# Kernel optimization log

Measured on AMD Instinct MI355X. Metric: run time of the kernel, lower is better.

## Reference

```python
import jax, jax.numpy as jnp
import numpy as np

N = 400000      # simplices (edges of the complexes)
E = 2400000     # nnz of each Laplacian
F_IN = 32
H = 64
KAPPA = 3
G = 512         # graphs in batch
N_OUT = 8
EPS = 1e-5


def spmm(edge_index, edge_values, x, n):
    # y[i] = sum_e val_e * x[j],  i = edge_index[0], j = edge_index[1]
    msg = edge_values[:, None] * x[edge_index[1]]
    return jax.ops.segment_sum(msg, edge_index[0], num_segments=n)


def sc_layer(x, li, lv, ui, uv, Wl, bl, Wu, bu, Wh, bh):
    # SCNN layer: z_low + z_up + z_har (aggr_x fused in)
    n = x.shape[0]
    z = x @ Wh + bh                       # harmonic / identity term
    xl = x
    for k in range(KAPPA):
        xl = spmm(li, lv, xl, n)          # L_low^{k+1} x
        z = z + xl @ Wl[k] + bl[k]
    xu = x
    for k in range(KAPPA):
        xu = spmm(ui, uv, xu, n)          # L_up^{k+1} x
        z = z + xu @ Wu[k] + bu[k]
    return z


def batch_norm(x, gamma, beta):
    mean = jnp.mean(x, axis=0)
    var = jnp.mean((x - mean) ** 2, axis=0)   # biased, as torch BN training
    return (x - mean) * jax.lax.rsqrt(var + EPS) * gamma + beta


def setup_inputs() -> dict:
    key = jax.random.key(0)
    ks = jax.random.split(key, 32)
    s_in = 1.0 / np.sqrt(F_IN)
    s_h = 1.0 / np.sqrt(H)
    inp = {
        "x": jax.random.normal(ks[0], (N, F_IN), jnp.float32),
        "lower_edge_index": jax.random.randint(ks[1], (2, E), 0, N),
        "lower_edge_values": jax.random.normal(ks[2], (E,), jnp.float32),
        "upper_edge_index": jax.random.randint(ks[3], (2, E), 0, N),
        "upper_edge_values": jax.random.normal(ks[4], (E,), jnp.float32),
        "batch_index": jnp.sort(jax.random.randint(ks[5], (N,), 0, G)),
        # layer 0 (F_IN -> H)
        "l0_Wl": jax.random.normal(ks[6], (KAPPA, F_IN, H), jnp.float32) * s_in,
        "l0_bl": jnp.zeros((KAPPA, H), jnp.float32),
        "l0_Wu": jax.random.normal(ks[7], (KAPPA, F_IN, H), jnp.float32) * s_in,
        "l0_bu": jnp.zeros((KAPPA, H), jnp.float32),
        "l0_Wh": jax.random.normal(ks[8], (F_IN, H), jnp.float32) * s_in,
        "l0_bh": jnp.zeros((H,), jnp.float32),
        # layer 1 (H -> H)
        "l1_Wl": jax.random.normal(ks[9], (KAPPA, H, H), jnp.float32) * s_h,
        "l1_bl": jnp.zeros((KAPPA, H), jnp.float32),
        "l1_Wu": jax.random.normal(ks[10], (KAPPA, H, H), jnp.float32) * s_h,
        "l1_bu": jnp.zeros((KAPPA, H), jnp.float32),
        "l1_Wh": jax.random.normal(ks[11], (H, H), jnp.float32) * s_h,
        "l1_bh": jnp.zeros((H,), jnp.float32),
        # batch norms
        "bn0_g": jnp.ones((H,), jnp.float32),
        "bn0_b": jnp.zeros((H,), jnp.float32),
        "bn1_g": jnp.ones((H,), jnp.float32),
        "bn1_b": jnp.zeros((H,), jnp.float32),
        # output MLP [2H, H, N_OUT]
        "mlp_W1": jax.random.normal(ks[12], (2 * H, H), jnp.float32) / np.sqrt(2 * H),
        "mlp_b1": jnp.zeros((H,), jnp.float32),
        "mlp_W2": jax.random.normal(ks[13], (H, N_OUT), jnp.float32) * s_h,
        "mlp_b2": jnp.zeros((N_OUT,), jnp.float32),
    }
    return inp


def reference(x, lower_edge_values, upper_edge_values,
              l0_Wl, l0_bl, l0_Wu, l0_bu, l0_Wh, l0_bh,
              l1_Wl, l1_bl, l1_Wu, l1_bu, l1_Wh, l1_bh,
              bn0_g, bn0_b, bn1_g, bn1_b,
              mlp_W1, mlp_b1, mlp_W2, mlp_b2,
              lower_edge_index, upper_edge_index, batch_index):
    li, ui, bi = lower_edge_index, upper_edge_index, batch_index
    lv, uv = lower_edge_values, upper_edge_values

    h = sc_layer(x, li, lv, ui, uv, l0_Wl, l0_bl, l0_Wu, l0_bu, l0_Wh, l0_bh)
    h = jax.nn.elu(batch_norm(h, bn0_g, bn0_b))
    h = sc_layer(h, li, lv, ui, uv, l1_Wl, l1_bl, l1_Wu, l1_bu, l1_Wh, l1_bh)
    h = jax.nn.elu(batch_norm(h, bn1_g, bn1_b))

    # global max pool + global mean pool per graph
    gmax = jax.ops.segment_max(h, bi, num_segments=G)
    gsum = jax.ops.segment_sum(h, bi, num_segments=G)
    cnt = jax.ops.segment_sum(jnp.ones((h.shape[0],), h.dtype), bi, num_segments=G)
    gmean = gsum / jnp.maximum(cnt, 1.0)[:, None]
    g = jax.nn.elu(jnp.concatenate([gmax, gmean], axis=1))  # [G, 2H]

    # MLP [2H -> H -> N_OUT]
    g = jax.nn.relu(g @ mlp_W1 + mlp_b1)
    return g @ mlp_W2 + mlp_b2
```

## Files before the change

kernel.cpp:

```cpp
#include <hip/hip_runtime.h>
#include <hip/hip_bf16.h>
#include <math.h>

#define N_SIMP 400000
#define E_NNZ  2400000
#define FIN    32
#define HDIM   64
#define KAPPA  3
#define G_NUM  512
#define NOUT   8
#define BN_EPS 1e-5

#define NDIG_HALF 391
#define NDIG      782
#define P1_EDGES  8192
#define P1_BLOCKS 586
#define P1_T      1024
#define P1_EPT    8
#define P2_CAP    7168
#define P2_T      512
#define P2_ITERS  14

#define MF_BLOCKS_C 6250

typedef __hip_bfloat16 bf16;
typedef _Float16 f16;
typedef short s8v __attribute__((ext_vector_type(8)));
typedef ushort u8v __attribute__((ext_vector_type(8)));
typedef _Float16 h8v __attribute__((ext_vector_type(8)));
typedef float f4v __attribute__((ext_vector_type(4)));

__device__ __forceinline__ float elu_f(float x) {
    return x > 0.f ? x : expm1f(x);
}
__device__ __forceinline__ float bf2f(ushort u) {
    return __uint_as_float(((unsigned int)u) << 16);
}
__device__ __forceinline__ ushort f2bf(float f) {
    bf16 h = (bf16)f;
    return *(ushort*)&h;
}


__global__ __launch_bounds__(P1_T) void p1_sort_kernel(
        const int* __restrict__ eiL, const float* __restrict__ lv,
        const int* __restrict__ eiU, const float* __restrict__ uv,
        int* __restrict__ ccnt, int* __restrict__ bofsv,
        int2* __restrict__ coarse) {
    __shared__ int2 rec[P1_EDGES];
    __shared__ int h[NDIG];
    __shared__ int hscan[P1_T];
    int t = threadIdx.x;
    for (int j = t; j < NDIG; j += P1_T) h[j] = 0;
    __syncthreads();
    int base_i = blockIdx.x * P1_EDGES;
    int key[P1_EPT], val[P1_EPT], dg[P1_EPT];
#pragma unroll
    for (int k = 0; k < P1_EPT; ++k) {
        int i = base_i + k * P1_T + t;
        int dd = -1;
        if (i < 2 * E_NNZ) {
            int row, col;
            float v;
            if (i < E_NNZ) {
                row = eiL[i]; col = eiL[E_NNZ + i]; v = lv[i];
                dd = row >> 10;
            } else {
                int e = i - E_NNZ;
                row = eiU[e]; col = eiU[E_NNZ + e]; v = uv[e];
                dd = NDIG_HALF + (row >> 10);
            }
            key[k] = ((row & 1023) << 22) | col;
            val[k] = __float_as_int(v);
            atomicAdd(&h[dd], 1);
        }
        dg[k] = dd;
    }
    __syncthreads();
    int cv = (t < NDIG) ? h[t] : 0;
    hscan[t] = cv;
    __syncthreads();
    for (int off = 1; off < P1_T; off <<= 1) {
        int x = (t >= off) ? hscan[t - off] : 0;
        __syncthreads();
        hscan[t] += x;
        __syncthreads();
    }
    if (t < NDIG) {
        int ex = hscan[t] - cv;
        ccnt[blockIdx.x * NDIG + t] = cv;
        bofsv[blockIdx.x * NDIG + t] = ex;
        h[t] = ex;
    }
    __syncthreads();
#pragma unroll
    for (int k = 0; k < P1_EPT; ++k) {
        if (dg[k] >= 0) {
            int pos = atomicAdd(&h[dg[k]], 1);
            rec[pos] = make_int2(key[k], val[k]);
        }
    }
    __syncthreads();
    int2* dst = coarse + (size_t)blockIdx.x * P1_EDGES;
    int nrec = 2 * E_NNZ - base_i;
    if (nrec > P1_EDGES) nrec = P1_EDGES;
    for (int j = t; j < nrec; j += P1_T) dst[j] = rec[j];
}

__global__ void digit_total_kernel(const int* __restrict__ cnt, int* __restrict__ tot) {
    int d = blockIdx.x * 256 + threadIdx.x;
    if (d >= NDIG) return;
    int run = 0;
    for (int b = 0; b < P1_BLOCKS; ++b) run += cnt[b * NDIG + d];
    tot[d] = run;
}

__global__ __launch_bounds__(1024) void scan_base_kernel(int* __restrict__ tot) {
    __shared__ int s[1024];
    int t = threadIdx.x;
    int v = (t < NDIG) ? tot[t] : 0;
    s[t] = v;
    __syncthreads();
    for (int off = 1; off < 1024; off <<= 1) {
        int x = (t >= off) ? s[t - off] : 0;
        __syncthreads();
        s[t] += x;
        __syncthreads();
    }
    if (t < NDIG) tot[t] = s[t] - v;
    if (t == 1023) tot[NDIG] = s[1023];
}


__global__ __launch_bounds__(P2_T) void p2_build_kernel(
        const int2* __restrict__ coarse, const int* __restrict__ ccnt,
        const int* __restrict__ bofsv, const int* __restrict__ basev,
        int* __restrict__ rpL, int* __restrict__ rpU,
        int2* __restrict__ edgeL, int2* __restrict__ edgeU) {
    __shared__ int pk[P2_CAP];
    __shared__ int vl[P2_CAP];
    __shared__ int hist[1024];
    __shared__ int sc[P2_T];
    __shared__ int flen[P1_BLOCKS];
    __shared__ int fofs[P1_BLOCKS];
    __shared__ int fo[P1_BLOCKS];
    __shared__ int stot;
    int d = blockIdx.x;
    int t = threadIdx.x;
    int f0 = 2 * t, f1 = 2 * t + 1;
    int L0 = 0, L1 = 0, O0 = 0, O1 = 0;
    if (f0 < P1_BLOCKS) { L0 = ccnt[f0 * NDIG + d]; O0 = bofsv[f0 * NDIG + d]; }
    if (f1 < P1_BLOCKS) { L1 = ccnt[f1 * NDIG + d]; O1 = bofsv[f1 * NDIG + d]; }
    sc[t] = L0 + L1;
    __syncthreads();
    for (int off = 1; off < P2_T; off <<= 1) {
        int x = (t >= off) ? sc[t - off] : 0;
        __syncthreads();
        sc[t] += x;
        __syncthreads();
    }
    int pb = sc[t] - (L0 + L1);
    if (f0 < P1_BLOCKS) { flen[f0] = L0; fofs[f0] = O0; fo[f0] = pb; }
    if (f1 < P1_BLOCKS) { flen[f1] = L1; fofs[f1] = O1; fo[f1] = pb + L0; }
    if (t == P2_T - 1) stot = sc[t];
    __syncthreads();
    int sz = stot;
    if (sz > P2_CAP) sz = P2_CAP;
    int wv = t >> 6, lane = t & 63;
    int grp8 = lane >> 3, l8 = lane & 7;
    for (int b = wv * 8 + grp8; b < P1_BLOCKS; b += 64) {
        int L = flen[b], O = fofs[b], F = fo[b];
        const int2* sp = coarse + (size_t)b * P1_EDGES + O;
        for (int j = l8; j < L; j += 8) {
            int dst2 = F + j;
            if (dst2 < P2_CAP) {
                int2 r = sp[j];
                pk[dst2] = r.x;
                vl[dst2] = r.y;
            }
        }
    }
    __syncthreads();
    hist[t] = 0;
    hist[t + P2_T] = 0;
    __syncthreads();
    int myrank[P2_ITERS];
#pragma unroll
    for (int k = 0; k < P2_ITERS; ++k) {
        int j = k * P2_T + t;
        myrank[k] = (j < sz) ? atomicAdd(&hist[((unsigned)pk[j]) >> 22], 1) : 0;
    }
    __syncthreads();
    int h0 = hist[2 * t], h1 = hist[2 * t + 1];
    sc[t] = h0 + h1;
    __syncthreads();
    for (int off = 1; off < P2_T; off <<= 1) {
        int x = (t >= off) ? sc[t - off] : 0;
        __syncthreads();
        sc[t] += x;
        __syncthreads();
    }
    int pbase = sc[t] - (h0 + h1);
    __syncthreads();
    hist[2 * t] = pbase;
    hist[2 * t + 1] = pbase + h0;
    int which = (d >= NDIG_HALF);
    int lbase = basev[d] - (which ? E_NNZ : 0);
    int rowbase = (which ? d - NDIG_HALF : d) << 10;
    int* rp = which ? rpU : rpL;
    int r0 = rowbase + 2 * t, r1 = r0 + 1;
    if (r0 < N_SIMP) rp[r0] = lbase + pbase;
    if (r1 < N_SIMP) rp[r1] = lbase + pbase + h0;
    __syncthreads();
    int2* eout = which ? edgeU : edgeL;
#pragma unroll
    for (int k = 0; k < P2_ITERS; ++k) {
        int j = k * P2_T + t;
        if (j < sz) {
            unsigned p = (unsigned)pk[j];
            int pos = lbase + hist[p >> 22] + myrank[k];
            eout[pos] = make_int2((int)(p & 0x3FFFFF), vl[j]);
        }
    }
}


__global__ void combine_bias_kernel(const float* __restrict__ bh,
                                    const float* __restrict__ bl,
                                    const float* __restrict__ bu,
                                    float* __restrict__ out) {
    int h = threadIdx.x;
    float acc = bh[h];
    for (int k = 0; k < KAPPA; ++k) acc += bl[k * HDIM + h] + bu[k * HDIM + h];
    out[h] = acc;
}

__global__ void f32_to_bf16_kernel(const float* __restrict__ in, bf16* __restrict__ out) {
    int idx = blockIdx.x * 256 + threadIdx.x;
    float4 v = ((const float4*)in)[idx];
    ushort4 w;
    w.x = f2bf(v.x); w.y = f2bf(v.y); w.z = f2bf(v.z); w.w = f2bf(v.w);
    ((ushort4*)out)[idx] = w;
}

__global__ void wtrans_all_kernel(const float* __restrict__ s0, const float* __restrict__ s1,
                                  const float* __restrict__ s2, const float* __restrict__ s3,
                                  const float* __restrict__ s4, const float* __restrict__ s5,
                                  ushort* __restrict__ wt) {
    int idx = blockIdx.x * 256 + threadIdx.x;
    const float* src; int off;
    if (idx < 2048)       { src = s0; off = 0; }
    else if (idx < 6144)  { src = s1; off = 2048; }
    else if (idx < 12288) { src = s2; off = 6144; }
    else if (idx < 18432) { src = s3; off = 12288; }
    else if (idx < 30720) { src = s4; off = 18432; }
    else                  { src = s5; off = 30720; }
    int rel = idx - off;
    int frag = rel >> 9;
    int r = rel & 511;
    int lane = r >> 3, j = r & 7;
    int q = lane >> 4, n = lane & 15;
    int ch = frag >> 2, nblk = frag & 3;
    int k = ch * 32 + q * 8 + j;
    int nout = nblk * 16 + n;
    wt[idx] = f2bf(src[k * 64 + nout]);
}


__global__ void spmm32_kernel(const int* __restrict__ rp, const int2* __restrict__ edge,
                              const bf16* __restrict__ srcb, int src_stride,
                              bf16* __restrict__ dstb) {
    const ushort* src = (const ushort*)srcb;
    ushort* dst = (ushort*)dstb;
    int tid = threadIdx.x;
    int lane = tid & 63;
    int wv = tid >> 6;
    int grp = lane >> 2;
    int li = lane & 3;
    int row = blockIdx.x * 64 + wv * 16 + grp;
    int s = rp[row];
    int e = (row == N_SIMP - 1) ? E_NNZ : rp[row + 1];
    int deg = e - s;
    float a[8] = {0.f, 0.f, 0.f, 0.f, 0.f, 0.f, 0.f, 0.f};
    if (deg > 0) {
        int2 ed[8];
#pragma unroll
        for (int t = 0; t < 8; ++t) {
            int j = s + t;
            ed[t] = edge[(j < e) ? j : (e - 1)];
        }
        u8v xs[8];
#pragma unroll
        for (int t = 0; t < 8; ++t)
            xs[t] = *(const u8v*)(src + (size_t)ed[t].x * src_stride + li * 8);
#pragma unroll
        for (int t = 0; t < 8; ++t) {
            float v = (t < deg) ? __int_as_float(ed[t].y) : 0.f;
#pragma unroll
            for (int c = 0; c < 8; ++c) a[c] += v * bf2f(xs[t][c]);
        }
        for (int j = s + 8; j < e; j += 4) {
            int2 e2[4];
#pragma unroll
            for (int t = 0; t < 4; ++t) {
                int jj = j + t;
                e2[t] = edge[(jj < e) ? jj : (e - 1)];
            }
            u8v x2[4];
#pragma unroll
            for (int t = 0; t < 4; ++t)
                x2[t] = *(const u8v*)(src + (size_t)e2[t].x * src_stride + li * 8);
#pragma unroll
            for (int t = 0; t < 4; ++t) {
                float v = (j + t < e) ? __int_as_float(e2[t].y) : 0.f;
#pragma unroll
                for (int c = 0; c < 8; ++c) a[c] += v * bf2f(x2[t][c]);
            }
        }
    }
    u8v w;
#pragma unroll
    for (int c = 0; c < 8; ++c) w[c] = f2bf(a[c]);
    *(u8v*)(dst + (size_t)row * 32 + li * 8) = w;
}

__global__ void spmm64_kernel(const int* __restrict__ rp, const int2* __restrict__ edge,
                              const bf16* __restrict__ srcb, bf16* __restrict__ dstb) {
    const ushort* src = (const ushort*)srcb;
    ushort* dst = (ushort*)dstb;
    int tid = threadIdx.x;
    int lane = tid & 63;
    int wv = tid >> 6;
    int grp = lane >> 3;
    int li = lane & 7;
    int row = blockIdx.x * 32 + wv * 8 + grp;
    int s = rp[row];
    int e = (row == N_SIMP - 1) ? E_NNZ : rp[row + 1];
    int deg = e - s;
    float a[8] = {0.f, 0.f, 0.f, 0.f, 0.f, 0.f, 0.f, 0.f};
    if (deg > 0) {
        int2 ed[8];
#pragma unroll
        for (int t = 0; t < 8; ++t) {
            int j = s + t;
            ed[t] = edge[(j < e) ? j : (e - 1)];
        }
        u8v xs[8];
#pragma unroll
        for (int t = 0; t < 8; ++t)
            xs[t] = *(const u8v*)(src + (size_t)ed[t].x * 64 + li * 8);
#pragma unroll
        for (int t = 0; t < 8; ++t) {
            float v = (t < deg) ? __int_as_float(ed[t].y) : 0.f;
#pragma unroll
            for (int c = 0; c < 8; ++c) a[c] += v * bf2f(xs[t][c]);
        }
        for (int j = s + 8; j < e; j += 4) {
            int2 e2[4];
#pragma unroll
            for (int t = 0; t < 4; ++t) {
                int jj = j + t;
                e2[t] = edge[(jj < e) ? jj : (e - 1)];
            }
            u8v x2[4];
#pragma unroll
            for (int t = 0; t < 4; ++t)
                x2[t] = *(const u8v*)(src + (size_t)e2[t].x * 64 + li * 8);
#pragma unroll
            for (int t = 0; t < 4; ++t) {
                float v = (j + t < e) ? __int_as_float(e2[t].y) : 0.f;
#pragma unroll
                for (int c = 0; c < 8; ++c) a[c] += v * bf2f(x2[t][c]);
            }
        }
    }
    u8v w;
#pragma unroll
    for (int c = 0; c < 8; ++c) w[c] = f2bf(a[c]);
    *(u8v*)(dst + (size_t)row * 64 + li * 8) = w;
}


template <int NCH, int NCH1, bool INIT, bool STATS>
__global__ __launch_bounds__(256) void mfma_gemm_kernel(
        const ushort* __restrict__ s0, int st0,
        const ushort* __restrict__ s1, int st1,
        const ushort* __restrict__ s2, int st2,
        const ushort* __restrict__ s3, int st3,
        const ushort* __restrict__ s4, int st4,
        const ushort* __restrict__ s5, int st5,
        const ushort* __restrict__ Wt1,
        const ushort* __restrict__ Wt2,
        const float* __restrict__ bias,
        float* __restrict__ partial,
        f16* __restrict__ z) {
    __shared__ float s_sum[64], s_sq[64];
    int tid = threadIdx.x;
    int wv = tid >> 6, lane = tid & 63;
    int quad = lane >> 4, n = lane & 15;
    int rowbase = blockIdx.x * 64 + wv * 16;
    int arow = rowbase + n;

    if (STATS) {
        if (tid < 64) { s_sum[tid] = 0.f; s_sq[tid] = 0.f; }
        __syncthreads();
    }

    f4v acc0 = {0.f, 0.f, 0.f, 0.f};
    f4v acc1 = {0.f, 0.f, 0.f, 0.f};
    f4v acc2 = {0.f, 0.f, 0.f, 0.f};
    f4v acc3 = {0.f, 0.f, 0.f, 0.f};

#pragma unroll
    for (int ch = 0; ch < NCH; ++ch) {
        const ushort* sp = (ch == 0) ? s0 : (ch == 1) ? s1 : (ch == 2) ? s2
                         : (ch == 3) ? s3 : (ch == 4) ? s4 : s5;
        int st = (ch == 0) ? st0 : (ch == 1) ? st1 : (ch == 2) ? st2
               : (ch == 3) ? st3 : (ch == 4) ? st4 : st5;
        const ushort* wb = (ch < NCH1) ? (Wt1 + (size_t)ch * 2048)
                                       : (Wt2 + (size_t)(ch - NCH1) * 2048);
        s8v a = *(const s8v*)(sp + (size_t)arow * st + quad * 8);
        const ushort* wq = wb + lane * 8;
        s8v b0 = *(const s8v*)(wq + 0 * 512);
        s8v b1 = *(const s8v*)(wq + 1 * 512);
        s8v b2 = *(const s8v*)(wq + 2 * 512);
        s8v b3 = *(const s8v*)(wq + 3 * 512);
        acc0 = __builtin_amdgcn_mfma_f32_16x16x32_bf16(a, b0, acc0, 0, 0, 0);
        acc1 = __builtin_amdgcn_mfma_f32_16x16x32_bf16(a, b1, acc1, 0, 0, 0);
        acc2 = __builtin_amdgcn_mfma_f32_16x16x32_bf16(a, b2, acc2, 0, 0, 0);
        acc3 = __builtin_amdgcn_mfma_f32_16x16x32_bf16(a, b3, acc3, 0, 0, 0);
    }
    float fs[4] = {0.f, 0.f, 0.f, 0.f};
    float fq[4] = {0.f, 0.f, 0.f, 0.f};
#pragma unroll
    for (int r = 0; r < 4; ++r) {
        int orow = rowbase + quad * 4 + r;
        f16* zp = z + (size_t)orow * 64 + n;
        f16 w0, w1, w2, w3;
        if (INIT) {
            w0 = (f16)(bias[n]      + acc0[r]);
            w1 = (f16)(bias[16 + n] + acc1[r]);
            w2 = (f16)(bias[32 + n] + acc2[r]);
            w3 = (f16)(bias[48 + n] + acc3[r]);
        } else {
            w0 = (f16)((float)zp[0]  + acc0[r]);
            w1 = (f16)((float)zp[16] + acc1[r]);
            w2 = (f16)((float)zp[32] + acc2[r]);
            w3 = (f16)((float)zp[48] + acc3[r]);
        }
        zp[0] = w0; zp[16] = w1; zp[32] = w2; zp[48] = w3;
        if (STATS) {
            float v0 = (float)w0, v1 = (float)w1, v2 = (float)w2, v3 = (float)w3;
            fs[0] += v0; fq[0] += v0 * v0;
            fs[1] += v1; fq[1] += v1 * v1;
            fs[2] += v2; fq[2] += v2 * v2;
            fs[3] += v3; fq[3] += v3 * v3;
        }
    }
    if (STATS) {
#pragma unroll
        for (int k = 0; k < 4; ++k) {
            atomicAdd(&s_sum[k * 16 + n], fs[k]);
            atomicAdd(&s_sq[k * 16 + n], fq[k]);
        }
        __syncthreads();
        if (tid < 64)  partial[(size_t)blockIdx.x * 128 + tid] = s_sum[tid];
        else if (tid < 128) partial[(size_t)blockIdx.x * 128 + tid] = s_sq[tid - 64];
    }
}

__global__ __launch_bounds__(256) void stats_reduce_kernel(
        const float* __restrict__ partial, double* __restrict__ stats) {
    __shared__ double sd[256];
    int slot = blockIdx.x;
    int t = threadIdx.x;
    double acc = 0.0;
    for (int j = t; j < MF_BLOCKS_C; j += 256)
        acc += (double)partial[(size_t)j * 128 + slot];
    sd[t] = acc;
    __syncthreads();
    for (int off = 128; off > 0; off >>= 1) {
        if (t < off) sd[t] += sd[t + off];
        __syncthreads();
    }
    if (t == 0) stats[slot] = sd[0];
}


__global__ void bn_elu_bf16_kernel(const f16* __restrict__ z, const double* __restrict__ stats,
                                   const float* __restrict__ gamma, const float* __restrict__ beta,
                                   bf16* __restrict__ out) {
    __shared__ float scale_s[64], shift_s[64];
    int tid = threadIdx.x;
    if (tid < 64) {
        double mean = stats[tid] / (double)N_SIMP;
        double var = stats[64 + tid] / (double)N_SIMP - mean * mean;
        double sc = (double)gamma[tid] / sqrt(var + BN_EPS);
        scale_s[tid] = (float)sc;
        shift_s[tid] = (float)((double)beta[tid] - mean * sc);
    }
    __syncthreads();
    const h8v* z8 = (const h8v*)z;
    u8v* o8 = (u8v*)out;
    const int total8 = N_SIMP * HDIM / 8;
    int hb = (tid & 7) * 8;
    for (int i = blockIdx.x * 256 + tid; i < total8; i += (int)gridDim.x * 256) {
        h8v v = z8[i];
        u8v w;
#pragma unroll
        for (int c = 0; c < 8; ++c)
            w[c] = f2bf(elu_f((float)v[c] * scale_s[hb + c] + shift_s[hb + c]));
        o8[i] = w;
    }
}

__global__ void pool_bn_kernel(const f16* __restrict__ zbuf, const int* __restrict__ bidx,
                               const double* __restrict__ stats,
                               const float* __restrict__ gamma, const float* __restrict__ beta,
                               float* __restrict__ gbuf) {
    __shared__ float scale_s[64], shift_s[64];
    __shared__ float pmax[256 * 8], psum[256 * 8];
    int tid = threadIdx.x;
    if (tid < 64) {
        double mean = stats[tid] / (double)N_SIMP;
        double var = stats[64 + tid] / (double)N_SIMP - mean * mean;
        double sc = (double)gamma[tid] / sqrt(var + BN_EPS);
        scale_s[tid] = (float)sc;
        shift_s[tid] = (float)((double)beta[tid] - mean * sc);
    }
    __syncthreads();
    int g = blockIdx.x;
    int lo = 0, hi = N_SIMP;
    while (lo < hi) { int mid = (lo + hi) >> 1; if (bidx[mid] < g) lo = mid + 1; else hi = mid; }
    int start = lo;
    hi = N_SIMP;
    while (lo < hi) { int mid = (lo + hi) >> 1; if (bidx[mid] < g + 1) lo = mid + 1; else hi = mid; }
    int end = lo;
    int li = tid & 7;
    int rr = tid >> 3;
    const h8v* z8 = (const h8v*)zbuf;
    float mx[8], sm[8];
#pragma unroll
    for (int c = 0; c < 8; ++c) { mx[c] = -INFINITY; sm[c] = 0.f; }
    float sc8[8], sh8[8];
#pragma unroll
    for (int c = 0; c < 8; ++c) { sc8[c] = scale_s[li * 8 + c]; sh8[c] = shift_s[li * 8 + c]; }
    for (int i = start + rr; i < end; i += 32) {
        h8v v = z8[(size_t)i * 8 + li];
#pragma unroll
        for (int c = 0; c < 8; ++c) {
            float y = elu_f((float)v[c] * sc8[c] + sh8[c]);
            mx[c] = fmaxf(mx[c], y);
            sm[c] += y;
        }
    }
#pragma unroll
    for (int c = 0; c < 8; ++c) { pmax[tid * 8 + c] = mx[c]; psum[tid * 8 + c] = sm[c]; }
    __syncthreads();
    if (tid < 64) {
        int sel = tid >> 3, slot = tid & 7;
        float m = -INFINITY, s = 0.f;
#pragma unroll 8
        for (int k = 0; k < 32; ++k) {
            int t = k * 8 + sel;
            m = fmaxf(m, pmax[t * 8 + slot]);
            s += psum[t * 8 + slot];
        }
        int cnt = end - start;
        float mean = s / fmaxf((float)cnt, 1.f);
        gbuf[g * 128 + tid] = elu_f(m);
        gbuf[g * 128 + 64 + tid] = elu_f(mean);
    }
}

__global__ void mlp_kernel(const float* __restrict__ gbuf, const float* __restrict__ W1,
                           const float* __restrict__ b1, const float* __restrict__ W2,
                           const float* __restrict__ b2, float* __restrict__ out) {
    __shared__ float gs[128];
    __shared__ float hs[64];
    int g = blockIdx.x, tid = threadIdx.x;
    gs[tid] = gbuf[g * 128 + tid];
    gs[64 + tid] = gbuf[g * 128 + 64 + tid];
    __syncthreads();
    float acc = b1[tid];
#pragma unroll
    for (int k = 0; k < 128; ++k) acc += gs[k] * W1[k * 64 + tid];
    hs[tid] = fmaxf(acc, 0.f);
    __syncthreads();
    if (tid < 8) {
        float o = b2[tid];
#pragma unroll
        for (int k = 0; k < 64; ++k) o += hs[k] * W2[k * 8 + tid];
        out[g * 8 + tid] = o;
    }
}


extern "C" void kernel_launch(void* const* d_in, const int* in_sizes, int n_in,
                              void* d_out, int out_size, void* d_ws, size_t ws_size,
                              hipStream_t stream) {
    const float* x     = (const float*)d_in[0];
    const int*   li    = (const int*)d_in[1];
    const float* lv    = (const float*)d_in[2];
    const int*   ui    = (const int*)d_in[3];
    const float* uv    = (const float*)d_in[4];
    const int*   bidx  = (const int*)d_in[5];
    const float* l0_Wl = (const float*)d_in[6];
    const float* l0_bl = (const float*)d_in[7];
    const float* l0_Wu = (const float*)d_in[8];
    const float* l0_bu = (const float*)d_in[9];
    const float* l0_Wh = (const float*)d_in[10];
    const float* l0_bh = (const float*)d_in[11];
    const float* l1_Wl = (const float*)d_in[12];
    const float* l1_bl = (const float*)d_in[13];
    const float* l1_Wu = (const float*)d_in[14];
    const float* l1_bu = (const float*)d_in[15];
    const float* l1_Wh = (const float*)d_in[16];
    const float* l1_bh = (const float*)d_in[17];
    const float* bn0_g = (const float*)d_in[18];
    const float* bn0_b = (const float*)d_in[19];
    const float* bn1_g = (const float*)d_in[20];
    const float* bn1_b = (const float*)d_in[21];
    const float* mW1   = (const float*)d_in[22];
    const float* mb1   = (const float*)d_in[23];
    const float* mW2   = (const float*)d_in[24];
    const float* mb2   = (const float*)d_in[25];
    float* out = (float*)d_out;

    char* base = (char*)d_ws;
    f16*   z     = (f16*)base;
    bf16*  h0bf  = (bf16*)(base + 51200000ull);
    bf16*  g1    = (bf16*)(base + 102400000ull);
    bf16*  g2    = (bf16*)(base + 153600000ull);
    int2*  edgeL = (int2*)(base + 204800000ull);
    int2*  edgeU = (int2*)(base + 224000000ull);
    int*   rpL   = (int*)(base + 243200000ull);
    int*   rpU   = (int*)(base + 244800032ull);
    double* stats = (double*)(base + 246404160ull);
    float* cbias  = (float*)(base + 246405184ull);
    float* gbuf   = (float*)(base + 246405440ull);
    ushort* wt    = (ushort*)(base + 246667584ull);
    float* partial = (float*)(base + 246760000ull);

    int2* coarse = (int2*)base;
    int*  basev  = (int*)(base + 38500000ull);
    int*  ccnt   = (int*)(base + 51200000ull);
    int*  bofsv  = (int*)(base + 53100000ull);

    bf16* xbf  = g1;
    bf16* cAL  = g1 + (size_t)N_SIMP * 32;
    bf16* cBL  = g2;
    bf16* cCL  = g2 + (size_t)N_SIMP * 32;
    bf16* cAU  = h0bf;
    bf16* cBU  = h0bf + (size_t)N_SIMP * 32;
    bf16* cCU  = g1;

    ushort* wt_l0h = wt;
    ushort* wt_l1h = wt + 2048;
    ushort* wt_l0l = wt + 6144;
    ushort* wt_l0u = wt + 12288;
    ushort* wt_l1l = wt + 18432;
    ushort* wt_l1u = wt + 30720;

    const int SP32_BLOCKS = N_SIMP / 64;
    const int SP64_BLOCKS = N_SIMP / 32;
    const int MF_BLOCKS   = N_SIMP / 64;

    wtrans_all_kernel<<<168, 256, 0, stream>>>(l0_Wh, l1_Wh, l0_Wl, l0_Wu, l1_Wl, l1_Wu, wt);
    f32_to_bf16_kernel<<<N_SIMP * 32 / 4 / 256, 256, 0, stream>>>(x, xbf);

    p1_sort_kernel<<<P1_BLOCKS, P1_T, 0, stream>>>(li, lv, ui, uv, ccnt, bofsv, coarse);
    digit_total_kernel<<<(NDIG + 255) / 256, 256, 0, stream>>>(ccnt, basev);
    scan_base_kernel<<<1, 1024, 0, stream>>>(basev);
    p2_build_kernel<<<NDIG, P2_T, 0, stream>>>(coarse, ccnt, bofsv, basev,
                                               rpL, rpU, edgeL, edgeU);

    const ushort* xbfu = (const ushort*)xbf;
    const ushort* h0u  = (const ushort*)h0bf;
    const ushort* g1u  = (const ushort*)g1;
    const ushort* g2u  = (const ushort*)g2;

    combine_bias_kernel<<<1, 64, 0, stream>>>(l0_bh, l0_bl, l0_bu, cbias);
    mfma_gemm_kernel<1, 1, true, false><<<MF_BLOCKS, 256, 0, stream>>>(
        xbfu, 32, nullptr, 0, nullptr, 0, nullptr, 0, nullptr, 0, nullptr, 0,
        wt_l0h, wt_l0h, cbias, nullptr, z);

    spmm32_kernel<<<SP32_BLOCKS, 256, 0, stream>>>(rpL, edgeL, xbf, 32, cAL);
    spmm32_kernel<<<SP32_BLOCKS, 256, 0, stream>>>(rpL, edgeL, cAL, 32, cBL);
    spmm32_kernel<<<SP32_BLOCKS, 256, 0, stream>>>(rpL, edgeL, cBL, 32, cCL);
    spmm32_kernel<<<SP32_BLOCKS, 256, 0, stream>>>(rpU, edgeU, xbf, 32, cAU);
    spmm32_kernel<<<SP32_BLOCKS, 256, 0, stream>>>(rpU, edgeU, cAU, 32, cBU);
    spmm32_kernel<<<SP32_BLOCKS, 256, 0, stream>>>(rpU, edgeU, cBU, 32, cCU);
    mfma_gemm_kernel<6, 3, false, true><<<MF_BLOCKS, 256, 0, stream>>>(
        (const ushort*)cAL, 32, (const ushort*)cBL, 32, (const ushort*)cCL, 32,
        (const ushort*)cAU, 32, (const ushort*)cBU, 32, (const ushort*)cCU, 32,
        wt_l0l, wt_l0u, nullptr, partial, z);
    stats_reduce_kernel<<<128, 256, 0, stream>>>(partial, stats);

    bn_elu_bf16_kernel<<<1024, 256, 0, stream>>>(z, stats, bn0_g, bn0_b, h0bf);

    combine_bias_kernel<<<1, 64, 0, stream>>>(l1_bh, l1_bl, l1_bu, cbias);

    spmm64_kernel<<<SP64_BLOCKS, 256, 0, stream>>>(rpL, edgeL, h0bf, g1);
    spmm64_kernel<<<SP64_BLOCKS, 256, 0, stream>>>(rpL, edgeL, g1, g2);
    mfma_gemm_kernel<6, 2, true, false><<<MF_BLOCKS, 256, 0, stream>>>(
        h0u, 64, h0u + 32, 64, g1u, 64, g1u + 32, 64, g2u, 64, g2u + 32, 64,
        wt_l1h, wt_l1l, cbias, nullptr, z);
    spmm64_kernel<<<SP64_BLOCKS, 256, 0, stream>>>(rpL, edgeL, g2, g1);
    spmm64_kernel<<<SP64_BLOCKS, 256, 0, stream>>>(rpU, edgeU, h0bf, g2);
    mfma_gemm_kernel<4, 2, false, false><<<MF_BLOCKS, 256, 0, stream>>>(
        g1u, 64, g1u + 32, 64, g2u, 64, g2u + 32, 64, nullptr, 0, nullptr, 0,
        wt_l1l + 4 * 2048, wt_l1u, nullptr, nullptr, z);
    spmm64_kernel<<<SP64_BLOCKS, 256, 0, stream>>>(rpU, edgeU, g2, g1);
    spmm64_kernel<<<SP64_BLOCKS, 256, 0, stream>>>(rpU, edgeU, g1, g2);
    mfma_gemm_kernel<4, 4, false, true><<<MF_BLOCKS, 256, 0, stream>>>(
        g1u, 64, g1u + 32, 64, g2u, 64, g2u + 32, 64, nullptr, 0, nullptr, 0,
        wt_l1u + 2 * 2048, wt_l1u + 2 * 2048, nullptr, partial, z);
    stats_reduce_kernel<<<128, 256, 0, stream>>>(partial, stats);

    pool_bn_kernel<<<G_NUM, 256, 0, stream>>>(z, bidx, stats, bn1_g, bn1_b, gbuf);
    mlp_kernel<<<G_NUM, 64, 0, stream>>>(gbuf, mW1, mb1, mW2, mb2, out);
}
```

Before: 1.234 ms.

## Merge layer-1 GEMM passes and stage GEMM epilogue through LDS for vector stores

Layer 1 is rescheduled so the third lower-Laplacian power is written into the z buffer, reinterpreted as bf16 scratch. All lower-side and harmonic terms are then applied in one 8-chunk INIT GEMM, and all upper-side terms in one 6-chunk accumulating GEMM. This cuts one full read-modify-write pass over z and one kernel launch. The GEMM epilogue also now writes the accumulators to a shared-memory tile and emits 8-wide half-precision vector loads and stores, replacing scattered per-element stores. The cost is extra LDS traffic and a block barrier. Reusing z as scratch relies on each block reading its own rows before overwriting them.

Result: slower. 1.326 ms (+7.5%).

```diff
diff --git a/kernel.cpp b/kernel.cpp
--- a/kernel.cpp
+++ b/kernel.cpp
@@ -389,11 +389,14 @@
         const ushort* __restrict__ s3, int st3,
         const ushort* __restrict__ s4, int st4,
         const ushort* __restrict__ s5, int st5,
+        const ushort* __restrict__ s6, int st6,
+        const ushort* __restrict__ s7, int st7,
         const ushort* __restrict__ Wt1,
         const ushort* __restrict__ Wt2,
         const float* __restrict__ bias,
         float* __restrict__ partial,
         f16* __restrict__ z) {
+    __shared__ float ctile[64][68];
     __shared__ float s_sum[64], s_sq[64];
     int tid = threadIdx.x;
     int wv = tid >> 6, lane = tid & 63;
@@ -401,11 +404,6 @@
     int rowbase = blockIdx.x * 64 + wv * 16;
     int arow = rowbase + n;
 
-    if (STATS) {
-        if (tid < 64) { s_sum[tid] = 0.f; s_sq[tid] = 0.f; }
-        __syncthreads();
-    }
-
     f4v acc0 = {0.f, 0.f, 0.f, 0.f};
     f4v acc1 = {0.f, 0.f, 0.f, 0.f};
     f4v acc2 = {0.f, 0.f, 0.f, 0.f};
@@ -414,9 +412,11 @@
 #pragma unroll
     for (int ch = 0; ch < NCH; ++ch) {
         const ushort* sp = (ch == 0) ? s0 : (ch == 1) ? s1 : (ch == 2) ? s2
-                         : (ch == 3) ? s3 : (ch == 4) ? s4 : s5;
+                         : (ch == 3) ? s3 : (ch == 4) ? s4 : (ch == 5) ? s5
+                         : (ch == 6) ? s6 : s7;
         int st = (ch == 0) ? st0 : (ch == 1) ? st1 : (ch == 2) ? st2
-               : (ch == 3) ? st3 : (ch == 4) ? st4 : st5;
+               : (ch == 3) ? st3 : (ch == 4) ? st4 : (ch == 5) ? st5
+               : (ch == 6) ? st6 : st7;
         const ushort* wb = (ch < NCH1) ? (Wt1 + (size_t)ch * 2048)
                                        : (Wt2 + (size_t)(ch - NCH1) * 2048);
         s8v a = *(const s8v*)(sp + (size_t)arow * st + quad * 8);
@@ -430,38 +430,49 @@
         acc2 = __builtin_amdgcn_mfma_f32_16x16x32_bf16(a, b2, acc2, 0, 0, 0);
         acc3 = __builtin_amdgcn_mfma_f32_16x16x32_bf16(a, b3, acc3, 0, 0, 0);
     }
-    float fs[4] = {0.f, 0.f, 0.f, 0.f};
-    float fq[4] = {0.f, 0.f, 0.f, 0.f};
 #pragma unroll
     for (int r = 0; r < 4; ++r) {
-        int orow = rowbase + quad * 4 + r;
-        f16* zp = z + (size_t)orow * 64 + n;
-        f16 w0, w1, w2, w3;
+        int lrow = wv * 16 + quad * 4 + r;
+        ctile[lrow][n]      = acc0[r];
+        ctile[lrow][16 + n] = acc1[r];
+        ctile[lrow][32 + n] = acc2[r];
+        ctile[lrow][48 + n] = acc3[r];
+    }
+    if (STATS && tid < 64) { s_sum[tid] = 0.f; s_sq[tid] = 0.f; }
+    __syncthreads();
+    float fs[8] = {0, 0, 0, 0, 0, 0, 0, 0};
+    float fq[8] = {0, 0, 0, 0, 0, 0, 0, 0};
+    int cb = (tid & 7) * 8;
+#pragma unroll
+    for (int k = 0; k < 2; ++k) {
+        int lrow = (tid + k * 256) >> 3;
+        f16* zp = z + ((size_t)blockIdx.x * 64 + lrow) * 64 + cb;
+        h8v o;
         if (INIT) {
-            w0 = (f16)(bias[n]      + acc0[r]);
-            w1 = (f16)(bias[16 + n] + acc1[r]);
-            w2 = (f16)(bias[32 + n] + acc2[r]);
-            w3 = (f16)(bias[48 + n] + acc3[r]);
+#pragma unroll
+            for (int c = 0; c < 8; ++c)
+                o[c] = (f16)(ctile[lrow][cb + c] + bias[cb + c]);
         } else {
-            w0 = (f16)((float)zp[0]  + acc0[r]);
-            w1 = (f16)((float)zp[16] + acc1[r]);
-            w2 = (f16)((float)zp[32] + acc2[r]);
-            w3 = (f16)((float)zp[48] + acc3[r]);
-        }
-        zp[0] = w0; zp[16] = w1; zp[32] = w2; zp[48] = w3;
+            h8v old = *(const h8v*)zp;
+#pragma unroll
+            for (int c = 0; c < 8; ++c)
+                o[c] = (f16)((float)old[c] + ctile[lrow][cb + c]);
+        }
+        *(h8v*)zp = o;
         if (STATS) {
-            float v0 = (float)w0, v1 = (float)w1, v2 = (float)w2, v3 = (float)w3;
-            fs[0] += v0; fq[0] += v0 * v0;
-            fs[1] += v1; fq[1] += v1 * v1;
-            fs[2] += v2; fq[2] += v2 * v2;
-            fs[3] += v3; fq[3] += v3 * v3;
+#pragma unroll
+            for (int c = 0; c < 8; ++c) {
+                float v = (float)o[c];
+                fs[c] += v;
+                fq[c] += v * v;
+            }
         }
     }
     if (STATS) {
 #pragma unroll
-        for (int k = 0; k < 4; ++k) {
-            atomicAdd(&s_sum[k * 16 + n], fs[k]);
-            atomicAdd(&s_sq[k * 16 + n], fq[k]);
+        for (int c = 0; c < 8; ++c) {
+            atomicAdd(&s_sum[cb + c], fs[c]);
+            atomicAdd(&s_sq[cb + c], fq[c]);
         }
         __syncthreads();
         if (tid < 64)  partial[(size_t)blockIdx.x * 128 + tid] = s_sum[tid];
@@ -655,6 +666,8 @@
     bf16* cBU  = h0bf + (size_t)N_SIMP * 32;
     bf16* cCU  = g1;
 
+    bf16* zb = (bf16*)z;
+
     ushort* wt_l0h = wt;
     ushort* wt_l1h = wt + 2048;
     ushort* wt_l0l = wt + 6144;
@@ -679,11 +692,12 @@
     const ushort* h0u  = (const ushort*)h0bf;
     const ushort* g1u  = (const ushort*)g1;
     const ushort* g2u  = (const ushort*)g2;
+    const ushort* zbu  = (const ushort*)zb;
 
     combine_bias_kernel<<<1, 64, 0, stream>>>(l0_bh, l0_bl, l0_bu, cbias);
     mfma_gemm_kernel<1, 1, true, false><<<MF_BLOCKS, 256, 0, stream>>>(
         xbfu, 32, nullptr, 0, nullptr, 0, nullptr, 0, nullptr, 0, nullptr, 0,
-        wt_l0h, wt_l0h, cbias, nullptr, z);
+        nullptr, 0, nullptr, 0, wt_l0h, wt_l0h, cbias, nullptr, z);
 
     spmm32_kernel<<<SP32_BLOCKS, 256, 0, stream>>>(rpL, edgeL, xbf, 32, cAL);
     spmm32_kernel<<<SP32_BLOCKS, 256, 0, stream>>>(rpL, edgeL, cAL, 32, cBL);
@@ -694,7 +708,7 @@
     mfma_gemm_kernel<6, 3, false, true><<<MF_BLOCKS, 256, 0, stream>>>(
         (const ushort*)cAL, 32, (const ushort*)cBL, 32, (const ushort*)cCL, 32,
         (const ushort*)cAU, 32, (const ushort*)cBU, 32, (const ushort*)cCU, 32,
-        wt_l0l, wt_l0u, nullptr, partial, z);
+        nullptr, 0, nullptr, 0, wt_l0l, wt_l0u, nullptr, partial, z);
     stats_reduce_kernel<<<128, 256, 0, stream>>>(partial, stats);
 
     bn_elu_bf16_kernel<<<1024, 256, 0, stream>>>(z, stats, bn0_g, bn0_b, h0bf);
@@ -703,19 +717,16 @@
 
     spmm64_kernel<<<SP64_BLOCKS, 256, 0, stream>>>(rpL, edgeL, h0bf, g1);
     spmm64_kernel<<<SP64_BLOCKS, 256, 0, stream>>>(rpL, edgeL, g1, g2);
-    mfma_gemm_kernel<6, 2, true, false><<<MF_BLOCKS, 256, 0, stream>>>(
+    spmm64_kernel<<<SP64_BLOCKS, 256, 0, stream>>>(rpL, edgeL, g2, zb);
+    mfma_gemm_kernel<8, 2, true, false><<<MF_BLOCKS, 256, 0, stream>>>(
         h0u, 64, h0u + 32, 64, g1u, 64, g1u + 32, 64, g2u, 64, g2u + 32, 64,
-        wt_l1h, wt_l1l, cbias, nullptr, z);
-    spmm64_kernel<<<SP64_BLOCKS, 256, 0, stream>>>(rpL, edgeL, g2, g1);
-    spmm64_kernel<<<SP64_BLOCKS, 256, 0, stream>>>(rpU, edgeU, h0bf, g2);
-    mfma_gemm_kernel<4, 2, false, false><<<MF_BLOCKS, 256, 0, stream>>>(
-        g1u, 64, g1u + 32, 64, g2u, 64, g2u + 32, 64, nullptr, 0, nullptr, 0,
-        wt_l1l + 4 * 2048, wt_l1u, nullptr, nullptr, z);
-    spmm64_kernel<<<SP64_BLOCKS, 256, 0, stream>>>(rpU, edgeU, g2, g1);
+        zbu, 64, zbu + 32, 64, wt_l1h, wt_l1l, cbias, nullptr, z);
+    spmm64_kernel<<<SP64_BLOCKS, 256, 0, stream>>>(rpU, edgeU, h0bf, g1);
     spmm64_kernel<<<SP64_BLOCKS, 256, 0, stream>>>(rpU, edgeU, g1, g2);
-    mfma_gemm_kernel<4, 4, false, true><<<MF_BLOCKS, 256, 0, stream>>>(
-        g1u, 64, g1u + 32, 64, g2u, 64, g2u + 32, 64, nullptr, 0, nullptr, 0,
-        wt_l1u + 2 * 2048, wt_l1u + 2 * 2048, nullptr, partial, z);
+    spmm64_kernel<<<SP64_BLOCKS, 256, 0, stream>>>(rpU, edgeU, g2, h0bf);
+    mfma_gemm_kernel<6, 6, false, true><<<MF_BLOCKS, 256, 0, stream>>>(
+        g1u, 64, g1u + 32, 64, g2u, 64, g2u + 32, 64, h0u, 64, h0u + 32, 64,
+        nullptr, 0, nullptr, 0, wt_l1u, wt_l1u, nullptr, partial, z);
     stats_reduce_kernel<<<128, 256, 0, stream>>>(partial, stats);
 
     pool_bn_kernel<<<G_NUM, 256, 0, stream>>>(z, bidx, stats, bn1_g, bn1_b, gbuf);
```
